# Optimization experiments

Hardware: AMD Instinct MI355X
Metric: run time of the kernel (lower is better)

Reference implementation:

```python
import jax, jax.numpy as jnp
import numpy as np
from jax import lax

SMOOTH = 1.0
CONVEX = 1.0
MAX_IT = 500  # eval=False path in legendre
TOL = 0.001
B, C, H = 1024, 64, 128


def _icnn(x, Wy0, by0, Wy1, by1, Wz1, Wy2, by2, Wz2):
    # ICNN: softplus chain with positive (clamped) Wz weights, plus strongly-convex quadratic term
    h = jax.nn.softplus(x @ Wy0.T + by0)                                   # [B, H]
    h = jax.nn.softplus(h @ jnp.clip(Wz1, 0.0, 1e10).T + x @ Wy1.T + by1)  # [B, H]
    out = jax.nn.softplus(h @ jnp.clip(Wz2, 0.0, 1e10).T + x @ Wy2.T + by2)  # [B, 1]
    return out + (1.0 / (2.0 * SMOOTH)) * jnp.sum(x * x, axis=1, keepdims=True)


def _legendre(z, Wy0, by0, Wy1, by1, Wz1, Wy2, by2, Wz2):
    # grad of per-sample scalar ICNN output w.r.t. its input (sum trick: outputs are sample-wise independent)
    grad_icnn = jax.grad(lambda xx: jnp.sum(_icnn(xx, Wy0, by0, Wy1, by1, Wz1, Wy2, by2, Wz2)))
    step = 2.0 * SMOOTH

    def body(carry, i):
        x1, done = carry
        g = grad_icnn(x1)
        new_x1 = x1 + (step / (i + 1.0)) * (z - g)
        x1 = jnp.where(done, x1, new_x1)
        err = jnp.mean(jnp.linalg.norm(z - g, axis=1))
        done = jnp.logical_or(done, err < TOL)
        return (x1, done), None

    x1_0 = jnp.ones_like(z)
    (x1, _), _ = lax.scan(body, (x1_0, jnp.array(False)), jnp.arange(MAX_IT, dtype=z.dtype))
    return x1 + CONVEX * z


def _xavier(key, shape):
    fan_out, fan_in = shape
    std = np.sqrt(2.0 / (fan_in + fan_out))
    return jax.random.normal(key, shape, dtype=jnp.float32) * std


def setup_inputs() -> dict:
    key = jax.random.key(0)
    ks = jax.random.split(key, 8)
    bound0 = 1.0 / np.sqrt(C)
    return {
        "x": jax.random.normal(ks[0], (B, C), dtype=jnp.float32),
        "Wy0": _xavier(ks[1], (H, C)),
        "by0": jax.random.uniform(ks[2], (H,), dtype=jnp.float32, minval=-bound0, maxval=bound0),
        "Wy1": _xavier(ks[3], (H, C)),
        "by1": jax.random.uniform(ks[4], (H,), dtype=jnp.float32, minval=-bound0, maxval=bound0),
        "Wz1": _xavier(ks[5], (H, H)),
        "Wy2": _xavier(ks[6], (1, C)),
        "by2": jax.random.uniform(ks[7], (1,), dtype=jnp.float32, minval=-bound0, maxval=bound0),
        "Wz2": _xavier(jax.random.fold_in(key, 99), (1, H)),
    }


def reference(x, Wy0, by0, Wy1, by1, Wz1, Wy2, by2, Wz2):
    return _legendre(x, Wy0, by0, Wy1, by1, Wz1, Wy2, by2, Wz2)
```

## Files before the change

kernel.cpp:

```cpp
#include <hip/hip_runtime.h>
#include <math.h>

#define NB 1024
#define NC 64
#define NH 128
#define MAX_IT 200
#define TOLF 6e-3f

typedef _Float16 f16x8 __attribute__((ext_vector_type(8)));
typedef float    f32x4 __attribute__((ext_vector_type(4)));
typedef _Float16 h2    __attribute__((ext_vector_type(2)));

#define MFMA(a, b, c) __builtin_amdgcn_mfma_f32_16x16x32_f16((a), (b), (c), 0, 0, 0)

__device__ __forceinline__ unsigned pack_h2(float a, float b) {
    union { h2 h; unsigned u; } cv;
    cv.h.x = (_Float16)a; cv.h.y = (_Float16)b; return cv.u;
}
__device__ __forceinline__ float rcp_fast(float x) {
#if __has_builtin(__builtin_amdgcn_rcpf)
    return __builtin_amdgcn_rcpf(x);
#else
    return 1.0f / x;
#endif
}
__device__ __forceinline__ void sigsp(float a, float& sig, float& sp) {
    const float e = __expf(-fabsf(a));
    const float r = rcp_fast(1.0f + e);
    sig = (a >= 0.0f) ? r : e * r;
    sp  = fmaxf(a, 0.0f) + __logf(1.0f + e);
}
__device__ __forceinline__ float sigm(float a) {
    const float e = __expf(-fabsf(a));
    const float r = rcp_fast(1.0f + e);
    return (a >= 0.0f) ? r : e * r;
}
__device__ __forceinline__ float clp(float x) { return fmaxf(x, 0.0f); }

__device__ __forceinline__ f16x8 ld8(const float* p) {
    const float4 a = ((const float4*)p)[0];
    const float4 b = ((const float4*)p)[1];
    f16x8 r;
    r[0]=(_Float16)a.x; r[1]=(_Float16)a.y; r[2]=(_Float16)a.z; r[3]=(_Float16)a.w;
    r[4]=(_Float16)b.x; r[5]=(_Float16)b.y; r[6]=(_Float16)b.z; r[7]=(_Float16)b.w;
    return r;
}
__device__ __forceinline__ f16x8 ld8_clip(const float* p) {
    const float4 a = ((const float4*)p)[0];
    const float4 b = ((const float4*)p)[1];
    f16x8 r;
    r[0]=(_Float16)clp(a.x); r[1]=(_Float16)clp(a.y); r[2]=(_Float16)clp(a.z); r[3]=(_Float16)clp(a.w);
    r[4]=(_Float16)clp(b.x); r[5]=(_Float16)clp(b.y); r[6]=(_Float16)clp(b.z); r[7]=(_Float16)clp(b.w);
    return r;
}
__device__ __forceinline__ f16x8 ld8_str(const float* p, int stride) {
    f16x8 r;
    #pragma unroll
    for (int j = 0; j < 8; ++j) r[j] = (_Float16)p[j * stride];
    return r;
}
__device__ __forceinline__ f16x8 ld8_str_clip(const float* p, int stride) {
    f16x8 r;
    #pragma unroll
    for (int j = 0; j < 8; ++j) r[j] = (_Float16)clp(p[j * stride]);
    return r;
}

__launch_bounds__(512, 1)
__global__ void blnn_kernel(const float* __restrict__ xin,
                            const float* __restrict__ Wy0,
                            const float* __restrict__ by0,
                            const float* __restrict__ Wy1,
                            const float* __restrict__ by1,
                            const float* __restrict__ Wz1,
                            const float* __restrict__ Wy2,
                            const float* __restrict__ by2,
                            const float* __restrict__ Wz2,
                            float* __restrict__ out)
{
    __shared__ __align__(16) _Float16 xact [4 * 80];
    __shared__ __align__(16) _Float16 h0act[4 * 144];
    __shared__ __align__(16) _Float16 v1act[4 * 144];
    __shared__ __align__(16) _Float16 v0act[4 * 144];
    __shared__ __align__(16) float hp[32];
    __shared__ __align__(16) float pxp[16];
    __shared__ __align__(16) float npar[16];

    const int tid  = threadIdx.x;
    const int w    = tid >> 6;
    const int cm   = w & 3;
    const int l    = tid & 63;
    const int n    = l & 15;
    const int n4   = n & 3;
    const int quad = l >> 4;
    const int blk4 = blockIdx.x * 4;

    const int rA = w * 16 + n;
    const int rT = cm * 16 + n;
    const int kq = quad * 8;

    f16x8 wa0[2], wa1[2];
    #pragma unroll
    for (int ks = 0; ks < 2; ++ks) {
        wa0[ks] = ld8(Wy0 + rA * 64 + ks * 32 + kq);
        wa1[ks] = ld8(Wy1 + rA * 64 + ks * 32 + kq);
    }
    f16x8 waz[4], wzt[4], w1t[4], w0t[4];
    #pragma unroll
    for (int ks = 0; ks < 4; ++ks) {
        waz[ks] = ld8_clip(Wz1 + rA * 128 + ks * 32 + kq);
        wzt[ks] = ld8_str_clip(Wz1 + (ks * 32 + kq) * 128 + rA, 128);
        w1t[ks] = ld8_str(Wy1 + (ks * 32 + kq) * 64 + rT, 64);
        w0t[ks] = ld8_str(Wy0 + (ks * 32 + kq) * 64 + rT, 64);
    }
    const float4 bb0 = *(const float4*)(by0 + w * 16 + quad * 4);
    const float4 bb1 = *(const float4*)(by1 + w * 16 + quad * 4);
    float4 wzq;
    {
        const float4 t = *(const float4*)(Wz2 + w * 16 + quad * 4);
        wzq.x = clp(t.x); wzq.y = clp(t.y); wzq.z = clp(t.z); wzq.w = clp(t.w);
    }

    if (tid < 256) {
        const int nn = tid >> 6, cc = tid & 63;
        xact[nn * 80 + cc] = (_Float16)xin[(blk4 + nn) * 64 + cc];
    }

    const float4 z4  = ((const float4*)xin)[(blk4 + n4) * 16 + cm * 4 + quad];
    const float4 wy4 = ((const float4*)Wy2)[cm * 4 + quad];
    float zr[4]   = {z4.x, z4.y, z4.z, z4.w};
    float wy2r[4] = {wy4.x, wy4.y, wy4.z, wy4.w};
    float xcur[4] = {zr[0], zr[1], zr[2], zr[3]};
    float lamE = 1.0f, prevn2 = 3.4e38f;
    const float b2 = by2[0];

    {
        float pxs = wy2r[0]*xcur[0] + wy2r[1]*xcur[1] + wy2r[2]*xcur[2] + wy2r[3]*xcur[3];
        pxs += __shfl_xor(pxs, 16, 64);
        pxs += __shfl_xor(pxs, 32, 64);
        if (w < 4 && l < 4) pxp[l * 4 + w] = pxs;
    }
    __syncthreads();

    const _Float16* xrow  = xact  + n4 * 80;
    const _Float16* h0row = h0act + n4 * 144;
    const _Float16* v1row = v1act + n4 * 144;
    const _Float16* v0row = v0act + n4 * 144;

    float sig0[4];

    for (int it = 0; it < MAX_IT; ++it) {
        f16x8 bx0 = *(const f16x8*)(xrow + quad * 8);
        f16x8 bx1 = *(const f16x8*)(xrow + 32 + quad * 8);
        {
            f32x4 acc = {0.f, 0.f, 0.f, 0.f};
            acc = MFMA(wa0[0], bx0, acc);
            acc = MFMA(wa0[1], bx1, acc);
            float sp0, sp1, sp2, sp3;
            sigsp(acc[0] + bb0.x, sig0[0], sp0);
            sigsp(acc[1] + bb0.y, sig0[1], sp1);
            sigsp(acc[2] + bb0.z, sig0[2], sp2);
            sigsp(acc[3] + bb0.w, sig0[3], sp3);
            if (n < 4)
                *(uint2*)&h0act[n4 * 144 + w * 16 + quad * 4] =
                    make_uint2(pack_h2(sp0, sp1), pack_h2(sp2, sp3));
        }
        __syncthreads();

        f16x8 bh0 = *(const f16x8*)(h0row + quad * 8);
        f16x8 bh1 = *(const f16x8*)(h0row + 32 + quad * 8);
        f16x8 bh2 = *(const f16x8*)(h0row + 64 + quad * 8);
        f16x8 bh3 = *(const f16x8*)(h0row + 96 + quad * 8);
        float hsum = 0.0f;
        {
            f32x4 acc = {0.f, 0.f, 0.f, 0.f};
            acc = MFMA(waz[0], bh0, acc);
            acc = MFMA(waz[1], bh1, acc);
            acc = MFMA(waz[2], bh2, acc);
            acc = MFMA(waz[3], bh3, acc);
            acc = MFMA(wa1[0], bx0, acc);
            acc = MFMA(wa1[1], bx1, acc);
            float s1, h1;
            sigsp(acc[0] + bb1.x, s1, h1); hsum = fmaf(wzq.x, h1, hsum);
            const float t0 = s1 * wzq.x;
            sigsp(acc[1] + bb1.y, s1, h1); hsum = fmaf(wzq.y, h1, hsum);
            const float t1 = s1 * wzq.y;
            sigsp(acc[2] + bb1.z, s1, h1); hsum = fmaf(wzq.z, h1, hsum);
            const float t2 = s1 * wzq.z;
            sigsp(acc[3] + bb1.w, s1, h1); hsum = fmaf(wzq.w, h1, hsum);
            const float t3 = s1 * wzq.w;
            if (n < 4)
                *(uint2*)&v1act[n4 * 144 + w * 16 + quad * 4] =
                    make_uint2(pack_h2(t0, t1), pack_h2(t2, t3));
        }
        hsum += __shfl_xor(hsum, 16, 64);
        hsum += __shfl_xor(hsum, 32, 64);
        if (l < 4) hp[l * 8 + w] = hsum;
        __syncthreads();

        float sg2c;
        {
            const float4 h0v = ((const float4*)hp)[n4 * 2];
            const float4 h1v = ((const float4*)hp)[n4 * 2 + 1];
            const float4 pv  = ((const float4*)pxp)[n4];
            sg2c = sigm(h0v.x + h0v.y + h0v.z + h0v.w +
                        h1v.x + h1v.y + h1v.z + h1v.w +
                        pv.x + pv.y + pv.z + pv.w + b2);
        }
        f16x8 bv10 = *(const f16x8*)(v1row + quad * 8);
        f16x8 bv11 = *(const f16x8*)(v1row + 32 + quad * 8);
        f16x8 bv12 = *(const f16x8*)(v1row + 64 + quad * 8);
        f16x8 bv13 = *(const f16x8*)(v1row + 96 + quad * 8);
        {
            f32x4 acc = {0.f, 0.f, 0.f, 0.f};
            acc = MFMA(wzt[0], bv10, acc);
            acc = MFMA(wzt[1], bv11, acc);
            acc = MFMA(wzt[2], bv12, acc);
            acc = MFMA(wzt[3], bv13, acc);
            const float a0 = sig0[0] * sg2c * acc[0];
            const float a1 = sig0[1] * sg2c * acc[1];
            const float a2 = sig0[2] * sg2c * acc[2];
            const float a3 = sig0[3] * sg2c * acc[3];
            if (n < 4)
                *(uint2*)&v0act[n4 * 144 + w * 16 + quad * 4] =
                    make_uint2(pack_h2(a0, a1), pack_h2(a2, a3));
        }
        f32x4 accg = {0.f, 0.f, 0.f, 0.f};
        accg = MFMA(w1t[0], bv10, accg);
        accg = MFMA(w1t[1], bv11, accg);
        accg = MFMA(w1t[2], bv12, accg);
        accg = MFMA(w1t[3], bv13, accg);
        __syncthreads();

        f16x8 bv00 = *(const f16x8*)(v0row + quad * 8);
        f16x8 bv01 = *(const f16x8*)(v0row + 32 + quad * 8);
        f16x8 bv02 = *(const f16x8*)(v0row + 64 + quad * 8);
        f16x8 bv03 = *(const f16x8*)(v0row + 96 + quad * 8);
        f32x4 acc0 = {0.f, 0.f, 0.f, 0.f};
        acc0 = MFMA(w0t[0], bv00, acc0);
        acc0 = MFMA(w0t[1], bv01, acc0);
        acc0 = MFMA(w0t[2], bv02, acc0);
        acc0 = MFMA(w0t[3], bv03, acc0);
        float resid[4];
        float r2 = 0.0f;
        #pragma unroll
        for (int r = 0; r < 4; ++r) {
            const float g = xcur[r] + sg2c * wy2r[r] + sg2c * accg[r] + acc0[r];
            resid[r] = zr[r] - g;
            r2 = fmaf(resid[r], resid[r], r2);
        }
        r2 += __shfl_xor(r2, 16, 64);
        r2 += __shfl_xor(r2, 32, 64);
        if (w < 4 && l < 4) npar[l * 4 + w] = r2;
        __syncthreads();

        const float4 q0 = ((const float4*)npar)[0];
        const float4 q1 = ((const float4*)npar)[1];
        const float4 q2 = ((const float4*)npar)[2];
        const float4 q3 = ((const float4*)npar)[3];
        const float s0 = q0.x + q0.y + q0.z + q0.w;
        const float s1 = q1.x + q1.y + q1.z + q1.w;
        const float s2 = q2.x + q2.y + q2.z + q2.w;
        const float s3 = q3.x + q3.y + q3.z + q3.w;
        const float T2 = TOLF * TOLF;
        if (s0 < T2 && s1 < T2 && s2 < T2 && s3 < T2) break;

        const float myn2 = (n4 == 0) ? s0 : (n4 == 1) ? s1 : (n4 == 2) ? s2 : s3;
        if (myn2 >= T2) {
            if (myn2 > prevn2 * 0.998f) lamE *= 0.5f;
            const float step = fmaxf(lamE, 1.0f / (float)(it + 2));
            #pragma unroll
            for (int r = 0; r < 4; ++r) xcur[r] = fmaf(step, resid[r], xcur[r]);
            prevn2 = myn2;
        }
        {
            float pxs = wy2r[0]*xcur[0] + wy2r[1]*xcur[1] + wy2r[2]*xcur[2] + wy2r[3]*xcur[3];
            pxs += __shfl_xor(pxs, 16, 64);
            pxs += __shfl_xor(pxs, 32, 64);
            if (w < 4 && l < 4) pxp[l * 4 + w] = pxs;
        }
        if (w < 4 && n < 4)
            *(uint2*)&xact[n4 * 80 + cm * 16 + quad * 4] =
                make_uint2(pack_h2(xcur[0], xcur[1]), pack_h2(xcur[2], xcur[3]));
        __syncthreads();
    }

    if (w < 4 && n < 4) {
        float4 o;
        o.x = xcur[0] + zr[0]; o.y = xcur[1] + zr[1];
        o.z = xcur[2] + zr[2]; o.w = xcur[3] + zr[3];
        ((float4*)out)[(blk4 + n4) * 16 + cm * 4 + quad] = o;
    }
}

extern "C" void kernel_launch(void* const* d_in, const int* in_sizes, int n_in,
                              void* d_out, int out_size, void* d_ws, size_t ws_size,
                              hipStream_t stream) {
    const float* xin = (const float*)d_in[0];
    const float* Wy0 = (const float*)d_in[1];
    const float* by0 = (const float*)d_in[2];
    const float* Wy1 = (const float*)d_in[3];
    const float* by1 = (const float*)d_in[4];
    const float* Wz1 = (const float*)d_in[5];
    const float* Wy2 = (const float*)d_in[6];
    const float* by2 = (const float*)d_in[7];
    const float* Wz2 = (const float*)d_in[8];
    float* out = (float*)d_out;

    blnn_kernel<<<dim3(NB / 4), dim3(512), 0, stream>>>(
        xin, Wy0, by0, Wy1, by1, Wz1, Wy2, by2, Wz2, out);
}
```

Before: 83.26 us.

## Split work into two-sample blocks of four waves, each wave owning two hidden tiles

Each block now handles 2 samples with 256 threads instead of 4 samples with 512, and the grid doubles. Each wave computes two 16-row hidden tiles, with register weight fragments doubled to match, and the launch bounds allow two blocks per CU. The aim is cheaper block barriers, since only 4 waves synchronise, and finer early-exit granularity, since each block stops once its own 2 samples converge. In exchange, each wave runs a longer serial MFMA chain, holds more registers, and repeats the hidden-layer MFMAs for fewer samples, wasting more of the 16-wide N dimension.

```diff
diff --git a/kernel.cpp b/kernel.cpp
--- a/kernel.cpp
+++ b/kernel.cpp
@@ -66,7 +66,7 @@
     return r;
 }
 
-__launch_bounds__(512, 1)
+__launch_bounds__(256, 2)
 __global__ void blnn_kernel(const float* __restrict__ xin,
                             const float* __restrict__ Wy0,
                             const float* __restrict__ by0,
@@ -78,56 +78,61 @@
                             const float* __restrict__ Wz2,
                             float* __restrict__ out)
 {
-    __shared__ __align__(16) _Float16 xact [4 * 80];
-    __shared__ __align__(16) _Float16 h0act[4 * 144];
-    __shared__ __align__(16) _Float16 v1act[4 * 144];
-    __shared__ __align__(16) _Float16 v0act[4 * 144];
-    __shared__ __align__(16) float hp[32];
-    __shared__ __align__(16) float pxp[16];
-    __shared__ __align__(16) float npar[16];
+    __shared__ __align__(16) _Float16 xact [2 * 80];
+    __shared__ __align__(16) _Float16 h0act[2 * 144];
+    __shared__ __align__(16) _Float16 v1act[2 * 144];
+    __shared__ __align__(16) _Float16 v0act[2 * 144];
+    __shared__ __align__(16) float hp[16];
+    __shared__ __align__(16) float pxp[8];
+    __shared__ __align__(16) float npar[8];
 
     const int tid  = threadIdx.x;
     const int w    = tid >> 6;
-    const int cm   = w & 3;
     const int l    = tid & 63;
     const int n    = l & 15;
-    const int n4   = n & 3;
+    const int n4   = n & 1;
     const int quad = l >> 4;
-    const int blk4 = blockIdx.x * 4;
-
-    const int rA = w * 16 + n;
-    const int rT = cm * 16 + n;
-    const int kq = quad * 8;
-
-    f16x8 wa0[2], wa1[2];
+    const int blk2 = blockIdx.x * 2;
+
+    const int rA0 = w * 32 + n;
+    const int rA1 = w * 32 + 16 + n;
+    const int rT  = w * 16 + n;
+    const int kq  = quad * 8;
+
+    f16x8 wa0[2][2], wa1[2][2];
     #pragma unroll
     for (int ks = 0; ks < 2; ++ks) {
-        wa0[ks] = ld8(Wy0 + rA * 64 + ks * 32 + kq);
-        wa1[ks] = ld8(Wy1 + rA * 64 + ks * 32 + kq);
-    }
-    f16x8 waz[4], wzt[4], w1t[4], w0t[4];
+        wa0[0][ks] = ld8(Wy0 + rA0 * 64 + ks * 32 + kq);
+        wa0[1][ks] = ld8(Wy0 + rA1 * 64 + ks * 32 + kq);
+        wa1[0][ks] = ld8(Wy1 + rA0 * 64 + ks * 32 + kq);
+        wa1[1][ks] = ld8(Wy1 + rA1 * 64 + ks * 32 + kq);
+    }
+    f16x8 waz[2][4], wzt[2][4], w1t[4], w0t[4];
     #pragma unroll
     for (int ks = 0; ks < 4; ++ks) {
-        waz[ks] = ld8_clip(Wz1 + rA * 128 + ks * 32 + kq);
-        wzt[ks] = ld8_str_clip(Wz1 + (ks * 32 + kq) * 128 + rA, 128);
-        w1t[ks] = ld8_str(Wy1 + (ks * 32 + kq) * 64 + rT, 64);
-        w0t[ks] = ld8_str(Wy0 + (ks * 32 + kq) * 64 + rT, 64);
-    }
-    const float4 bb0 = *(const float4*)(by0 + w * 16 + quad * 4);
-    const float4 bb1 = *(const float4*)(by1 + w * 16 + quad * 4);
-    float4 wzq;
-    {
-        const float4 t = *(const float4*)(Wz2 + w * 16 + quad * 4);
-        wzq.x = clp(t.x); wzq.y = clp(t.y); wzq.z = clp(t.z); wzq.w = clp(t.w);
-    }
-
-    if (tid < 256) {
+        waz[0][ks] = ld8_clip(Wz1 + rA0 * 128 + ks * 32 + kq);
+        waz[1][ks] = ld8_clip(Wz1 + rA1 * 128 + ks * 32 + kq);
+        wzt[0][ks] = ld8_str_clip(Wz1 + (ks * 32 + kq) * 128 + rA0, 128);
+        wzt[1][ks] = ld8_str_clip(Wz1 + (ks * 32 + kq) * 128 + rA1, 128);
+        w1t[ks]    = ld8_str(Wy1 + (ks * 32 + kq) * 64 + rT, 64);
+        w0t[ks]    = ld8_str(Wy0 + (ks * 32 + kq) * 64 + rT, 64);
+    }
+    float4 bb0[2], bb1[2], wzq[2];
+    #pragma unroll
+    for (int i = 0; i < 2; ++i) {
+        bb0[i] = *(const float4*)(by0 + (w * 2 + i) * 16 + quad * 4);
+        bb1[i] = *(const float4*)(by1 + (w * 2 + i) * 16 + quad * 4);
+        const float4 t = *(const float4*)(Wz2 + (w * 2 + i) * 16 + quad * 4);
+        wzq[i].x = clp(t.x); wzq[i].y = clp(t.y); wzq[i].z = clp(t.z); wzq[i].w = clp(t.w);
+    }
+
+    if (tid < 128) {
         const int nn = tid >> 6, cc = tid & 63;
-        xact[nn * 80 + cc] = (_Float16)xin[(blk4 + nn) * 64 + cc];
-    }
-
-    const float4 z4  = ((const float4*)xin)[(blk4 + n4) * 16 + cm * 4 + quad];
-    const float4 wy4 = ((const float4*)Wy2)[cm * 4 + quad];
+        xact[nn * 80 + cc] = (_Float16)xin[(blk2 + nn) * 64 + cc];
+    }
+
+    const float4 z4  = ((const float4*)xin)[(blk2 + n4) * 16 + w * 4 + quad];
+    const float4 wy4 = ((const float4*)Wy2)[w * 4 + quad];
     float zr[4]   = {z4.x, z4.y, z4.z, z4.w};
     float wy2r[4] = {wy4.x, wy4.y, wy4.z, wy4.w};
     float xcur[4] = {zr[0], zr[1], zr[2], zr[3]};
@@ -138,7 +143,7 @@
         float pxs = wy2r[0]*xcur[0] + wy2r[1]*xcur[1] + wy2r[2]*xcur[2] + wy2r[3]*xcur[3];
         pxs += __shfl_xor(pxs, 16, 64);
         pxs += __shfl_xor(pxs, 32, 64);
-        if (w < 4 && l < 4) pxp[l * 4 + w] = pxs;
+        if (l < 2) pxp[l * 4 + w] = pxs;
     }
     __syncthreads();
 
@@ -147,22 +152,24 @@
     const _Float16* v1row = v1act + n4 * 144;
     const _Float16* v0row = v0act + n4 * 144;
 
-    float sig0[4];
+    float sig0[2][4];
+    const float T2 = TOLF * TOLF;
 
     for (int it = 0; it < MAX_IT; ++it) {
         f16x8 bx0 = *(const f16x8*)(xrow + quad * 8);
         f16x8 bx1 = *(const f16x8*)(xrow + 32 + quad * 8);
-        {
+        #pragma unroll
+        for (int i = 0; i < 2; ++i) {
             f32x4 acc = {0.f, 0.f, 0.f, 0.f};
-            acc = MFMA(wa0[0], bx0, acc);
-            acc = MFMA(wa0[1], bx1, acc);
+            acc = MFMA(wa0[i][0], bx0, acc);
+            acc = MFMA(wa0[i][1], bx1, acc);
             float sp0, sp1, sp2, sp3;
-            sigsp(acc[0] + bb0.x, sig0[0], sp0);
-            sigsp(acc[1] + bb0.y, sig0[1], sp1);
-            sigsp(acc[2] + bb0.z, sig0[2], sp2);
-            sigsp(acc[3] + bb0.w, sig0[3], sp3);
-            if (n < 4)
-                *(uint2*)&h0act[n4 * 144 + w * 16 + quad * 4] =
+            sigsp(acc[0] + bb0[i].x, sig0[i][0], sp0);
+            sigsp(acc[1] + bb0[i].y, sig0[i][1], sp1);
+            sigsp(acc[2] + bb0[i].z, sig0[i][2], sp2);
+            sigsp(acc[3] + bb0[i].w, sig0[i][3], sp3);
+            if (n < 2)
+                *(uint2*)&h0act[n4 * 144 + (w * 2 + i) * 16 + quad * 4] =
                     make_uint2(pack_h2(sp0, sp1), pack_h2(sp2, sp3));
         }
         __syncthreads();
@@ -171,31 +178,38 @@
         f16x8 bh1 = *(const f16x8*)(h0row + 32 + quad * 8);
         f16x8 bh2 = *(const f16x8*)(h0row + 64 + quad * 8);
         f16x8 bh3 = *(const f16x8*)(h0row + 96 + quad * 8);
-        float hsum = 0.0f;
-        {
+        float hsum[2];
+        #pragma unroll
+        for (int i = 0; i < 2; ++i) {
             f32x4 acc = {0.f, 0.f, 0.f, 0.f};
-            acc = MFMA(waz[0], bh0, acc);
-            acc = MFMA(waz[1], bh1, acc);
-            acc = MFMA(waz[2], bh2, acc);
-            acc = MFMA(waz[3], bh3, acc);
-            acc = MFMA(wa1[0], bx0, acc);
-            acc = MFMA(wa1[1], bx1, acc);
-            float s1, h1;
-            sigsp(acc[0] + bb1.x, s1, h1); hsum = fmaf(wzq.x, h1, hsum);
-            const float t0 = s1 * wzq.x;
-            sigsp(acc[1] + bb1.y, s1, h1); hsum = fmaf(wzq.y, h1, hsum);
-            const float t1 = s1 * wzq.y;
-            sigsp(acc[2] + bb1.z, s1, h1); hsum = fmaf(wzq.z, h1, hsum);
-            const float t2 = s1 * wzq.z;
-            sigsp(acc[3] + bb1.w, s1, h1); hsum = fmaf(wzq.w, h1, hsum);
-            const float t3 = s1 * wzq.w;
-            if (n < 4)
-                *(uint2*)&v1act[n4 * 144 + w * 16 + quad * 4] =
+            acc = MFMA(waz[i][0], bh0, acc);
+            acc = MFMA(waz[i][1], bh1, acc);
+            acc = MFMA(waz[i][2], bh2, acc);
+            acc = MFMA(waz[i][3], bh3, acc);
+            acc = MFMA(wa1[i][0], bx0, acc);
+            acc = MFMA(wa1[i][1], bx1, acc);
+            float s1, h1, hs = 0.0f;
+            sigsp(acc[0] + bb1[i].x, s1, h1); hs = fmaf(wzq[i].x, h1, hs);
+            const float t0 = s1 * wzq[i].x;
+            sigsp(acc[1] + bb1[i].y, s1, h1); hs = fmaf(wzq[i].y, h1, hs);
+            const float t1 = s1 * wzq[i].y;
+            sigsp(acc[2] + bb1[i].z, s1, h1); hs = fmaf(wzq[i].z, h1, hs);
+            const float t2 = s1 * wzq[i].z;
+            sigsp(acc[3] + bb1[i].w, s1, h1); hs = fmaf(wzq[i].w, h1, hs);
+            const float t3 = s1 * wzq[i].w;
+            hsum[i] = hs;
+            if (n < 2)
+                *(uint2*)&v1act[n4 * 144 + (w * 2 + i) * 16 + quad * 4] =
                     make_uint2(pack_h2(t0, t1), pack_h2(t2, t3));
         }
-        hsum += __shfl_xor(hsum, 16, 64);
-        hsum += __shfl_xor(hsum, 32, 64);
-        if (l < 4) hp[l * 8 + w] = hsum;
+        hsum[0] += __shfl_xor(hsum[0], 16, 64);
+        hsum[0] += __shfl_xor(hsum[0], 32, 64);
+        hsum[1] += __shfl_xor(hsum[1], 16, 64);
+        hsum[1] += __shfl_xor(hsum[1], 32, 64);
+        if (l < 2) {
+            hp[l * 8 + w * 2 + 0] = hsum[0];
+            hp[l * 8 + w * 2 + 1] = hsum[1];
+        }
         __syncthreads();
 
         float sg2c;
@@ -211,18 +225,19 @@
         f16x8 bv11 = *(const f16x8*)(v1row + 32 + quad * 8);
         f16x8 bv12 = *(const f16x8*)(v1row + 64 + quad * 8);
         f16x8 bv13 = *(const f16x8*)(v1row + 96 + quad * 8);
-        {
+        #pragma unroll
+        for (int i = 0; i < 2; ++i) {
             f32x4 acc = {0.f, 0.f, 0.f, 0.f};
-            acc = MFMA(wzt[0], bv10, acc);
-            acc = MFMA(wzt[1], bv11, acc);
-            acc = MFMA(wzt[2], bv12, acc);
-            acc = MFMA(wzt[3], bv13, acc);
-            const float a0 = sig0[0] * sg2c * acc[0];
-            const float a1 = sig0[1] * sg2c * acc[1];
-            const float a2 = sig0[2] * sg2c * acc[2];
-            const float a3 = sig0[3] * sg2c * acc[3];
-            if (n < 4)
-                *(uint2*)&v0act[n4 * 144 + w * 16 + quad * 4] =
+            acc = MFMA(wzt[i][0], bv10, acc);
+            acc = MFMA(wzt[i][1], bv11, acc);
+            acc = MFMA(wzt[i][2], bv12, acc);
+            acc = MFMA(wzt[i][3], bv13, acc);
+            const float a0 = sig0[i][0] * sg2c * acc[0];
+            const float a1 = sig0[i][1] * sg2c * acc[1];
+            const float a2 = sig0[i][2] * sg2c * acc[2];
+            const float a3 = sig0[i][3] * sg2c * acc[3];
+            if (n < 2)
+                *(uint2*)&v0act[n4 * 144 + (w * 2 + i) * 16 + quad * 4] =
                     make_uint2(pack_h2(a0, a1), pack_h2(a2, a3));
         }
         f32x4 accg = {0.f, 0.f, 0.f, 0.f};
@@ -251,21 +266,16 @@
         }
         r2 += __shfl_xor(r2, 16, 64);
         r2 += __shfl_xor(r2, 32, 64);
-        if (w < 4 && l < 4) npar[l * 4 + w] = r2;
+        if (l < 2) npar[l * 4 + w] = r2;
         __syncthreads();
 
         const float4 q0 = ((const float4*)npar)[0];
         const float4 q1 = ((const float4*)npar)[1];
-        const float4 q2 = ((const float4*)npar)[2];
-        const float4 q3 = ((const float4*)npar)[3];
         const float s0 = q0.x + q0.y + q0.z + q0.w;
         const float s1 = q1.x + q1.y + q1.z + q1.w;
-        const float s2 = q2.x + q2.y + q2.z + q2.w;
-        const float s3 = q3.x + q3.y + q3.z + q3.w;
-        const float T2 = TOLF * TOLF;
-        if (s0 < T2 && s1 < T2 && s2 < T2 && s3 < T2) break;
-
-        const float myn2 = (n4 == 0) ? s0 : (n4 == 1) ? s1 : (n4 == 2) ? s2 : s3;
+        if (s0 < T2 && s1 < T2) break;
+
+        const float myn2 = (n4 == 0) ? s0 : s1;
         if (myn2 >= T2) {
             if (myn2 > prevn2 * 0.998f) lamE *= 0.5f;
             const float step = fmaxf(lamE, 1.0f / (float)(it + 2));
@@ -277,19 +287,19 @@
             float pxs = wy2r[0]*xcur[0] + wy2r[1]*xcur[1] + wy2r[2]*xcur[2] + wy2r[3]*xcur[3];
             pxs += __shfl_xor(pxs, 16, 64);
             pxs += __shfl_xor(pxs, 32, 64);
-            if (w < 4 && l < 4) pxp[l * 4 + w] = pxs;
-        }
-        if (w < 4 && n < 4)
-            *(uint2*)&xact[n4 * 80 + cm * 16 + quad * 4] =
+            if (l < 2) pxp[l * 4 + w] = pxs;
+        }
+        if (n < 2)
+            *(uint2*)&xact[n4 * 80 + w * 16 + quad * 4] =
                 make_uint2(pack_h2(xcur[0], xcur[1]), pack_h2(xcur[2], xcur[3]));
         __syncthreads();
     }
 
-    if (w < 4 && n < 4) {
+    if (n < 2) {
         float4 o;
         o.x = xcur[0] + zr[0]; o.y = xcur[1] + zr[1];
         o.z = xcur[2] + zr[2]; o.w = xcur[3] + zr[3];
-        ((float4*)out)[(blk4 + n4) * 16 + cm * 4 + quad] = o;
+        ((float4*)out)[(blk2 + n4) * 16 + w * 4 + quad] = o;
     }
 }
 
@@ -307,6 +317,6 @@
     const float* Wz2 = (const float*)d_in[8];
     float* out = (float*)d_out;
 
-    blnn_kernel<<<dim3(NB / 4), dim3(512), 0, stream>>>(
+    blnn_kernel<<<dim3(NB / 2), dim3(256), 0, stream>>>(
         xin, Wy0, by0, Wy1, by1, Wz1, Wy2, by2, Wz2, out);
 }
```

Measured after the change: 104.5 us. 1.26x slower.
